# Performance work log

Measured on AMD Instinct MI355X. Metric: run time of the kernel, lower is better.

The kernel has to match this reference:

```python
import jax, jax.numpy as jnp
import numpy as np

M = 4096      # dictionary_size
D = 64        # feature dim
YD = 4        # output dim (y_dim)
FF = 0.999    # forgetting_factor
REG = 1e-2    # regularisation
JITTER = 1e-10
LS = 8.0      # RBF lengthscale


def rbf(a, b):
    # squared-distance RBF Gram via the ||a||^2 + ||b||^2 - 2ab^T identity
    a2 = jnp.sum(a * a, -1)[:, None]
    b2 = jnp.sum(b * b, -1)[None, :]
    d2 = jnp.maximum(a2 + b2 - 2.0 * (a @ b.T), 0.0)
    return jnp.exp(-d2 / (2.0 * LS * LS))


def setup_inputs() -> dict:
    key = jax.random.key(0)
    ks = jax.random.split(key, 7)
    return {
        'dictionary': jax.random.normal(ks[0], (M, D), jnp.float32),
        'mu': jax.random.normal(ks[1], (YD, M, 1), jnp.float32),
        'sigma': jax.random.normal(ks[2], (M, M), jnp.float32),
        'Q': jax.random.normal(ks[3], (M, M), jnp.float32),
        'x': jax.random.normal(ks[4], (D,), jnp.float32),
        'y': jax.random.normal(ks[5], (YD,), jnp.float32),
        'noise_num': jax.random.uniform(ks[6], (YD, 1, 1), jnp.float32),
        'noise_den': jnp.ones((1,), jnp.float32),
        'time_index': jnp.arange(M, dtype=jnp.float32),
        't': M,
    }


def reference(dictionary, mu, sigma, Q, x, y, noise_num, noise_den, time_index, t):
    alloc = time_index >= 0.0                      # (M,) bool: allocated slots
    y_ = y[:, None, None]                          # (YD,1,1)

    # --- B2P forgetting ---
    Kdd = rbf(dictionary, dictionary) * (alloc[:, None] * alloc[None, :])
    sig = FF * sigma + (1.0 - FF) * Kdd
    mu_f = jnp.sqrt(FF) * mu

    # --- kernel evals for new sample ---
    K_dx = rbf(dictionary, x[None, :]) * alloc[:, None]   # (M,1)
    K_xx = rbf(x[None, :], x[None, :]) + JITTER           # (1,1)

    q_ = Q @ K_dx                                         # (M,1)
    pu = jnp.maximum(K_xx - K_dx.T @ q_, 0.0)             # projection uncertainty (1,1)
    h_ = sig @ q_                                         # (M,1)
    npv = jnp.maximum(pu + q_.T @ h_, 0.0)                # noiseless predictive var (1,1)
    pred_mean = q_.T @ mu_f                               # (YD,1,1) via batched matmul
    pv = REG + npv

    # --- augmented (M+1) state ---
    p_ = jnp.concatenate((h_, npv), axis=-2)              # (M+1,1)
    mu_a = jnp.concatenate((mu_f, pred_mean), axis=-2) + (y_ - pred_mean) / pv * p_
    sig_a = jnp.block([[sig, h_], [h_.T, npv]]) - (p_ @ p_.T) / pv
    p2 = jnp.concatenate((q_, -jnp.ones((1, 1), q_.dtype)), axis=0)
    Q_a = jnp.pad(Q, ((0, 1), (0, 1))) + (p2 @ p2.T) / pu

    nnum = noise_num + FF * (y_ - pred_mean) ** 2 / pv
    nden = noise_den + FF

    # --- pruning criterion ---
    x_alloc = jnp.concatenate((alloc, jnp.ones((1,), bool)))

    def crit_low(_):
        return jnp.concatenate((jnp.ones((M, 1), Q_a.dtype), jnp.zeros((1, 1), Q_a.dtype)))

    def crit_mse(_):
        dq = jnp.where(~x_alloc, jnp.inf, jnp.diag(Q_a))
        errors = Q_a @ mu_a / dq[:, None]                 # (YD,M+1,1)
        return jnp.abs(errors).sum(-3)                    # (M+1,1)

    criterion = jax.lax.cond(pu.squeeze() < JITTER, crit_low, crit_mse, None)
    prune = jnp.argmin(criterion)
    denom = jnp.where(~x_alloc[prune], jnp.inf, Q_a[prune, prune])

    # swap (prune <-> last) permutation, then drop last row/col
    perm = jnp.arange(M + 1)
    perm = jnp.where(perm == prune, M, jnp.where(perm == M, prune, perm))

    Q_r = Q_a[perm, :]                                    # row swap
    Qs = Q_r[:-1, prune]                                  # column `prune` after row swap
    Q_n = Q_r[:, perm][:M, :M] - jnp.outer(Qs, Qs) / denom

    mu_n = mu_a[:, perm, :][:, :M, :]
    sig_n = sig_a[perm, :][:, perm][:M, :M]

    dict_n = dictionary.at[prune].set(x)
    ti_n = time_index.at[prune].set(jnp.asarray(t, time_index.dtype))
    alloc_n = ti_n >= 0.0
    sig_n = (alloc_n[:, None] * alloc_n[None, :]) * sig_n
    mu_n = jnp.where((ti_n < 0.0)[:, None], 0.0, mu_n)

    return (mu_n, sig_n, Q_n, dict_n, ti_n, nnum, nden)
```

## Files before the change

kernel.cpp:

```cpp
#include <hip/hip_runtime.h>
#include <math.h>

#define Mn 4096
#define Dn 64
#define MUA_STRIDE 4104

#define OFF_A2   0
#define OFF_CRIT 0
#define OFF_K    4096
#define OFF_Q    8192
#define OFF_H    12288
#define OFF_MUA  16384
#define OFF_QS   32800
#define OFF_QSD  36896
#define SC_PU    40992
#define SC_INVPU 40993
#define SC_NPV   40994
#define SC_PV    40995
#define SC_INVPV 40996
#define SC_DENOM 40997
#define SC_PRUNE 40998

#define O_MU   0
#define O_SIG  16384
#define O_Q    16793600
#define O_DICT 33570816
#define O_TI   33832960
#define O_NNUM 33837056
#define O_NDEN 33837060

__device__ __forceinline__ float waveReduceSum(float v) {
#pragma unroll
    for (int o = 32; o > 0; o >>= 1) v += __shfl_down(v, o);
    return v;
}

__global__ void k1_prep(const float* __restrict__ dict, const float* __restrict__ x,
                        const float* __restrict__ ti, float* __restrict__ ws) {
    int row  = blockIdx.x * 4 + (threadIdx.x >> 6);
    int lane = threadIdx.x & 63;
    float d  = dict[row * Dn + lane];
    float xv = x[lane];
    float a2 = waveReduceSum(d * d);
    float x2 = waveReduceSum(xv * xv);
    float dx = waveReduceSum(d * xv);
    if (lane == 0) {
        ws[OFF_A2 + row] = a2;
        float d2 = fmaxf(a2 + x2 - 2.0f * dx, 0.0f);
        float kv = expf(d2 * (-1.0f / 128.0f));
        ws[OFF_K + row] = (ti[row] >= 0.0f) ? kv : 0.0f;
    }
}

__global__ void k2_q(const float* __restrict__ Q, float* __restrict__ ws) {
    __shared__ float red[4];
    const int row = blockIdx.x;
    const int tid = threadIdx.x;
    const float4* Qr = (const float4*)(Q + (size_t)row * Mn);
    const float4* kv = (const float4*)(ws + OFF_K);
    float s = 0.0f;
#pragma unroll
    for (int it = 0; it < 4; ++it) {
        int u = tid + it * 256;
        float4 a = Qr[u], b = kv[u];
        s += a.x * b.x + a.y * b.y + a.z * b.z + a.w * b.w;
    }
    s = waveReduceSum(s);
    if ((tid & 63) == 0) red[tid >> 6] = s;
    __syncthreads();
    if (tid == 0) {
        ws[OFF_Q + row] = red[0] + red[1] + red[2] + red[3];
        ws[OFF_H + row] = 0.0f;
    }
}

__global__ __launch_bounds__(256, 4) void k3_sig_h(
        const float* __restrict__ dict, const float* __restrict__ sigma,
        const float* __restrict__ ti, float* __restrict__ ws, float* __restrict__ out) {
    __shared__ __align__(16) float At[64 * 68];
    __shared__ __align__(16) float Bt[64 * 68];
    __shared__ float hred[64 * 16];
    const int tid = threadIdx.x;
    const int tx = tid & 15, ty = tid >> 4;
    const int r0 = blockIdx.y * 64;
    const int cchunk = blockIdx.x * 256;
    const int pidx = ((tid & 15) << 4) | (tid >> 4);

#pragma unroll
    for (int l = 0; l < 4; ++l) {
        int u = pidx + l * 256;
        int row = u >> 4;
        int col = (u & 15) << 2;
        float4 v = *(const float4*)(dict + (size_t)(r0 + row) * Dn + col);
        At[(col + 0) * 68 + row] = v.x;
        At[(col + 1) * 68 + row] = v.y;
        At[(col + 2) * 68 + row] = v.z;
        At[(col + 3) * 68 + row] = v.w;
    }

    float a2i[4], ali[4];
#pragma unroll
    for (int r = 0; r < 4; ++r) {
        int gi = r0 + ty * 4 + r;
        a2i[r] = ws[OFF_A2 + gi];
        ali[r] = (ti[gi] >= 0.0f) ? 1.0f : 0.0f;
    }

    float hacc[4] = {0.f, 0.f, 0.f, 0.f};

    for (int ct = 0; ct < 4; ++ct) {
        const int c0 = cchunk + ct * 64;
        __syncthreads();
#pragma unroll
        for (int l = 0; l < 4; ++l) {
            int u = pidx + l * 256;
            int row = u >> 4;
            int col = (u & 15) << 2;
            float4 v = *(const float4*)(dict + (size_t)(c0 + row) * Dn + col);
            Bt[(col + 0) * 68 + row] = v.x;
            Bt[(col + 1) * 68 + row] = v.y;
            Bt[(col + 2) * 68 + row] = v.z;
            Bt[(col + 3) * 68 + row] = v.w;
        }
        __syncthreads();

        float acc[4][4];
#pragma unroll
        for (int r = 0; r < 4; ++r)
#pragma unroll
            for (int c = 0; c < 4; ++c) acc[r][c] = 0.0f;

#pragma unroll
        for (int kk = 0; kk < 64; ++kk) {
            float4 av = *(const float4*)(At + kk * 68 + (ty << 2));
            float4 bv = *(const float4*)(Bt + kk * 68 + (tx << 2));
            acc[0][0] = fmaf(av.x, bv.x, acc[0][0]);
            acc[0][1] = fmaf(av.x, bv.y, acc[0][1]);
            acc[0][2] = fmaf(av.x, bv.z, acc[0][2]);
            acc[0][3] = fmaf(av.x, bv.w, acc[0][3]);
            acc[1][0] = fmaf(av.y, bv.x, acc[1][0]);
            acc[1][1] = fmaf(av.y, bv.y, acc[1][1]);
            acc[1][2] = fmaf(av.y, bv.z, acc[1][2]);
            acc[1][3] = fmaf(av.y, bv.w, acc[1][3]);
            acc[2][0] = fmaf(av.z, bv.x, acc[2][0]);
            acc[2][1] = fmaf(av.z, bv.y, acc[2][1]);
            acc[2][2] = fmaf(av.z, bv.z, acc[2][2]);
            acc[2][3] = fmaf(av.z, bv.w, acc[2][3]);
            acc[3][0] = fmaf(av.w, bv.x, acc[3][0]);
            acc[3][1] = fmaf(av.w, bv.y, acc[3][1]);
            acc[3][2] = fmaf(av.w, bv.z, acc[3][2]);
            acc[3][3] = fmaf(av.w, bv.w, acc[3][3]);
        }

        const int j = c0 + tx * 4;
        const float4 a2j4 = *(const float4*)(ws + OFF_A2 + j);
        const float4 qj4  = *(const float4*)(ws + OFF_Q + j);
        const float4 tj4  = *(const float4*)(ti + j);
        float a2j[4] = {a2j4.x, a2j4.y, a2j4.z, a2j4.w};
        float qj[4]  = {qj4.x, qj4.y, qj4.z, qj4.w};
        float alj[4] = {tj4.x >= 0.f ? 1.f : 0.f, tj4.y >= 0.f ? 1.f : 0.f,
                        tj4.z >= 0.f ? 1.f : 0.f, tj4.w >= 0.f ? 1.f : 0.f};

#pragma unroll
        for (int r = 0; r < 4; ++r) {
            const int gi = r0 + ty * 4 + r;
            const size_t off = (size_t)gi * Mn + j;
            const float4 sg = *(const float4*)(sigma + off);
            float sv[4] = {sg.x, sg.y, sg.z, sg.w};
            float res[4];
#pragma unroll
            for (int c = 0; c < 4; ++c) {
                float d2 = fmaxf(a2i[r] + a2j[c] - 2.0f * acc[r][c], 0.0f);
                float kv = __expf(d2 * (-1.0f / 128.0f)) * ali[r] * alj[c];
                res[c] = 0.999f * sv[c] + 0.001f * kv;
                hacc[r] += res[c] * qj[c];
            }
            float4 o = {res[0], res[1], res[2], res[3]};
            *(float4*)(out + O_SIG + off) = o;
        }
    }

    __syncthreads();
#pragma unroll
    for (int r = 0; r < 4; ++r) hred[(ty * 4 + r) * 16 + tx] = hacc[r];
    __syncthreads();
    if (tid < 64) {
        float s = 0.0f;
#pragma unroll
        for (int c = 0; c < 16; ++c) s += hred[tid * 16 + c];
        atomicAdd(ws + OFF_H + r0 + tid, s);
    }
}

__device__ __forceinline__ float blockReduce1024(float v, float* sred) {
    v = waveReduceSum(v);
    int tid = threadIdx.x;
    __syncthreads();
    if ((tid & 63) == 0) sred[tid >> 6] = v;
    __syncthreads();
    float r = 0.0f;
    if (tid == 0) {
#pragma unroll
        for (int i = 0; i < 16; ++i) r += sred[i];
    }
    return r;
}

__global__ __launch_bounds__(1024) void k4_scalars(
        const float* __restrict__ mu, const float* __restrict__ y,
        const float* __restrict__ nn, const float* __restrict__ nd,
        float* __restrict__ ws, float* __restrict__ out) {
    __shared__ float sred[16];
    __shared__ float sb[8];
    const int tid = threadIdx.x;
    const float* k = ws + OFF_K;
    const float* q = ws + OFF_Q;
    const float* h = ws + OFF_H;
    float kq = 0, qh = 0, p0 = 0, p1 = 0, p2 = 0, p3 = 0;
    for (int i = tid; i < Mn; i += 1024) {
        float qi = q[i];
        kq += k[i] * qi;
        qh += qi * h[i];
        p0 += qi * mu[0 * Mn + i];
        p1 += qi * mu[1 * Mn + i];
        p2 += qi * mu[2 * Mn + i];
        p3 += qi * mu[3 * Mn + i];
    }
    float rkq = blockReduce1024(kq, sred);
    float rqh = blockReduce1024(qh, sred);
    float r0 = blockReduce1024(p0, sred);
    float r1 = blockReduce1024(p1, sred);
    float r2 = blockReduce1024(p2, sred);
    float r3 = blockReduce1024(p3, sred);
    if (tid == 0) {
        const float sf = sqrtf(0.999f);
        float pu  = fmaxf(1.0f - rkq, 0.0f);
        float npv = fmaxf(pu + rqh, 0.0f);
        float pv  = 0.01f + npv;
        ws[SC_PU] = pu;
        ws[SC_INVPU] = 1.0f / pu;
        ws[SC_NPV] = npv;
        ws[SC_PV] = pv;
        ws[SC_INVPV] = 1.0f / pv;
        float pm[4] = {sf * r0, sf * r1, sf * r2, sf * r3};
#pragma unroll
        for (int yd = 0; yd < 4; ++yd) {
            float yv = y[yd];
            float dy = yv - pm[yd];
            float dl = dy / pv;
            sb[yd] = dl;
            ws[OFF_MUA + yd * MUA_STRIDE + Mn] = pm[yd] + dl * npv;
            out[O_NNUM + yd] = nn[yd] + 0.999f * (dy * dy) / pv;
        }
        out[O_NDEN] = nd[0] + 0.999f;
    }
    __syncthreads();
    const float sf = sqrtf(0.999f);
    float d0 = sb[0], d1 = sb[1], d2 = sb[2], d3 = sb[3];
    for (int i = tid; i < Mn; i += 1024) {
        float hi = h[i];
        ws[OFF_MUA + 0 * MUA_STRIDE + i] = sf * mu[0 * Mn + i] + d0 * hi;
        ws[OFF_MUA + 1 * MUA_STRIDE + i] = sf * mu[1 * Mn + i] + d1 * hi;
        ws[OFF_MUA + 2 * MUA_STRIDE + i] = sf * mu[2 * Mn + i] + d2 * hi;
        ws[OFF_MUA + 3 * MUA_STRIDE + i] = sf * mu[3 * Mn + i] + d3 * hi;
    }
}

__global__ __launch_bounds__(256) void k5_crit(const float* __restrict__ Q,
                                               const float* __restrict__ ti,
                                               float* __restrict__ ws) {
    __shared__ float sred[4][4];
    const int row = blockIdx.x;
    const int tid = threadIdx.x;
    const float pu = ws[SC_PU];
    if (pu < 1e-10f) {
        if (tid == 0) ws[OFF_CRIT + row] = (row < Mn) ? 1.0f : 0.0f;
        return;
    }
    const float inv_pu = ws[SC_INVPU];
    const bool rin = (row < Mn);
    const float p2i = rin ? ws[OFF_Q + row] : -1.0f;
    const float4* q4  = (const float4*)(ws + OFF_Q);
    const float4* Qr4 = (const float4*)(Q + (size_t)row * Mn);
    const float* mua = ws + OFF_MUA;
    float n0 = 0, n1 = 0, n2 = 0, n3 = 0;
#pragma unroll
    for (int it = 0; it < 4; ++it) {
        int u = tid + it * 256;
        float4 qv = q4[u];
        float4 base = rin ? Qr4[u] : make_float4(0.f, 0.f, 0.f, 0.f);
        float4 qa;
        qa.x = base.x + p2i * qv.x * inv_pu;
        qa.y = base.y + p2i * qv.y * inv_pu;
        qa.z = base.z + p2i * qv.z * inv_pu;
        qa.w = base.w + p2i * qv.w * inv_pu;
        const float4 m0 = *(const float4*)(mua + 0 * MUA_STRIDE + u * 4);
        const float4 m1 = *(const float4*)(mua + 1 * MUA_STRIDE + u * 4);
        const float4 m2 = *(const float4*)(mua + 2 * MUA_STRIDE + u * 4);
        const float4 m3 = *(const float4*)(mua + 3 * MUA_STRIDE + u * 4);
        n0 += qa.x * m0.x + qa.y * m0.y + qa.z * m0.z + qa.w * m0.w;
        n1 += qa.x * m1.x + qa.y * m1.y + qa.z * m1.z + qa.w * m1.w;
        n2 += qa.x * m2.x + qa.y * m2.y + qa.z * m2.z + qa.w * m2.w;
        n3 += qa.x * m3.x + qa.y * m3.y + qa.z * m3.z + qa.w * m3.w;
    }
    n0 = waveReduceSum(n0);
    n1 = waveReduceSum(n1);
    n2 = waveReduceSum(n2);
    n3 = waveReduceSum(n3);
    if ((tid & 63) == 0) {
        int w = tid >> 6;
        sred[w][0] = n0; sred[w][1] = n1; sred[w][2] = n2; sred[w][3] = n3;
    }
    __syncthreads();
    if (tid == 0) {
        float t0 = 0, t1 = 0, t2 = 0, t3 = 0;
#pragma unroll
        for (int w = 0; w < 4; ++w) {
            t0 += sred[w][0]; t1 += sred[w][1]; t2 += sred[w][2]; t3 += sred[w][3];
        }
        float qaM = -p2i * inv_pu;
        t0 += qaM * mua[0 * MUA_STRIDE + Mn];
        t1 += qaM * mua[1 * MUA_STRIDE + Mn];
        t2 += qaM * mua[2 * MUA_STRIDE + Mn];
        t3 += qaM * mua[3 * MUA_STRIDE + Mn];
        bool xa = rin ? (ti[row] >= 0.0f) : true;
        float crit = 0.0f;
        if (xa) {
            float dq = rin ? (Q[(size_t)row * Mn + row] + p2i * p2i * inv_pu) : inv_pu;
            crit = fabsf(t0 / dq) + fabsf(t1 / dq) + fabsf(t2 / dq) + fabsf(t3 / dq);
        }
        ws[OFF_CRIT + row] = crit;
    }
}

__global__ __launch_bounds__(1024) void k6_argmin(const float* __restrict__ Q,
                                                  const float* __restrict__ ti,
                                                  float* __restrict__ ws) {
    __shared__ float sval[1024];
    __shared__ int   sidx[1024];
    const int tid = threadIdx.x;
    float bv = INFINITY;
    int bi = Mn + 1;
    for (int i = tid; i <= Mn; i += 1024) {
        float v = ws[OFF_CRIT + i];
        if (v < bv) { bv = v; bi = i; }
    }
    sval[tid] = bv; sidx[tid] = bi;
    __syncthreads();
    for (int s = 512; s > 0; s >>= 1) {
        if (tid < s) {
            float ov = sval[tid + s]; int oi = sidx[tid + s];
            if (ov < sval[tid] || (ov == sval[tid] && oi < sidx[tid])) {
                sval[tid] = ov; sidx[tid] = oi;
            }
        }
        __syncthreads();
    }
    if (tid == 0) {
        int prune = sidx[0];
        ((int*)ws)[SC_PRUNE] = prune;
        float inv_pu = ws[SC_INVPU];
        bool xa = (prune == Mn) ? true : (ti[prune] >= 0.0f);
        float qap;
        if (prune < Mn) {
            float qp = ws[OFF_Q + prune];
            qap = Q[(size_t)prune * Mn + prune] + qp * qp * inv_pu;
        } else {
            qap = inv_pu;
        }
        ws[SC_DENOM] = xa ? qap : INFINITY;
    }
}

__global__ void k6b_vec(const float* __restrict__ Q, const float* __restrict__ dict,
                        const float* __restrict__ x, const float* __restrict__ ti,
                        const int* __restrict__ tptr, float* __restrict__ ws,
                        float* __restrict__ out) {
    const int tid = blockIdx.x * 256 + threadIdx.x;
    const int prune = ((const int*)ws)[SC_PRUNE];
    const int row = tid >> 6, col = tid & 63;
    out[O_DICT + tid] = (row == prune) ? x[col] : dict[tid];
    if (tid < Mn) {
        float tv = ti[tid];
        if (tid == prune) {
            int raw = *tptr;
            tv = (raw >= 0 && raw < (1 << 30)) ? (float)raw : __int_as_float(raw);
        }
        out[O_TI + tid] = tv;
        const float inv_pu = ws[SC_INVPU];
        const float denom  = ws[SC_DENOM];
        const float p2p = (prune < Mn) ? ws[OFF_Q + prune] : -1.0f;
        float qs;
        if (tid == prune) {
            qs = -p2p * inv_pu;
        } else {
            float base = (prune < Mn) ? Q[(size_t)tid * Mn + prune] : 0.0f;
            qs = base + ws[OFF_Q + tid] * p2p * inv_pu;
        }
        ws[OFF_QS + tid] = qs;
        ws[OFF_QSD + tid] = qs / denom;
    }
}

__global__ void k7_qn(const float* __restrict__ Q, float* __restrict__ out,
                      const float* __restrict__ ws) {
    const int i = blockIdx.x;
    const int tid = threadIdx.x;
    const int prune = ((const int*)ws)[SC_PRUNE];
    const float inv_pu = ws[SC_INVPU];
    const int pi = (i == prune) ? Mn : i;
    const bool piok = (pi < Mn);
    const float p2i = piok ? ws[OFF_Q + pi] : -1.0f;
    const float qsi = ws[OFF_QS + i];
    const float4* Qr4  = (const float4*)(Q + (size_t)pi * Mn);
    const float4* q4   = (const float4*)(ws + OFF_Q);
    const float4* qsd4 = (const float4*)(ws + OFF_QSD);
    float4* o4 = (float4*)(out + O_Q + (size_t)i * Mn);
#pragma unroll
    for (int it = 0; it < 4; ++it) {
        int u = tid + it * 256;
        float4 base = piok ? Qr4[u] : make_float4(0.f, 0.f, 0.f, 0.f);
        float4 p2j = q4[u];
        if ((prune >> 2) == u) {
            int c = prune & 3;
            ((float*)&p2j)[c] = -1.0f;
            ((float*)&base)[c] = 0.0f;
        }
        float4 d = qsd4[u];
        float4 r;
        r.x = base.x + p2i * p2j.x * inv_pu - qsi * d.x;
        r.y = base.y + p2i * p2j.y * inv_pu - qsi * d.y;
        r.z = base.z + p2i * p2j.z * inv_pu - qsi * d.z;
        r.w = base.w + p2i * p2j.w * inv_pu - qsi * d.w;
        o4[u] = r;
    }
}

__global__ void k8_sign(float* __restrict__ out, const float* __restrict__ ws) {
    const int i = blockIdx.x;
    const int tid = threadIdx.x;
    const int prune = ((const int*)ws)[SC_PRUNE];
    const float inv_pv = ws[SC_INVPV];
    const float npv = ws[SC_NPV];
    const bool ip = (i == prune);
    const float ai = (out[O_TI + i] >= 0.0f) ? 1.0f : 0.0f;
    const float hi = ws[OFF_H + i];
    const float p_i = ip ? npv : hi;
    const float4* h4  = (const float4*)(ws + OFF_H);
    const float4* ti4 = (const float4*)(out + O_TI);
    float4* s4 = (float4*)(out + O_SIG + (size_t)i * Mn);
#pragma unroll
    for (int it = 0; it < 4; ++it) {
        int u = tid + it * 256;
        float4 sv = s4[u];
        float4 hj = h4[u];
        float4 tv = ti4[u];
        float pj[4] = {hj.x, hj.y, hj.z, hj.w};
        float bs[4];
        if (ip) { bs[0] = hj.x; bs[1] = hj.y; bs[2] = hj.z; bs[3] = hj.w; }
        else    { bs[0] = sv.x; bs[1] = sv.y; bs[2] = sv.z; bs[3] = sv.w; }
        if ((prune >> 2) == u) {
            int c = prune & 3;
            pj[c] = npv;
            bs[c] = ip ? npv : hi;
        }
        float aj[4] = {tv.x >= 0.f ? 1.f : 0.f, tv.y >= 0.f ? 1.f : 0.f,
                       tv.z >= 0.f ? 1.f : 0.f, tv.w >= 0.f ? 1.f : 0.f};
        float4 r;
        r.x = ai * aj[0] * (bs[0] - p_i * pj[0] * inv_pv);
        r.y = ai * aj[1] * (bs[1] - p_i * pj[1] * inv_pv);
        r.z = ai * aj[2] * (bs[2] - p_i * pj[2] * inv_pv);
        r.w = ai * aj[3] * (bs[3] - p_i * pj[3] * inv_pv);
        s4[u] = r;
    }
}

__global__ void k9_mun(float* __restrict__ out, const float* __restrict__ ws) {
    const int idx = blockIdx.x * 256 + threadIdx.x;
    const int prune = ((const int*)ws)[SC_PRUNE];
    const int yd = idx >> 12;
    const int i  = idx & (Mn - 1);
    float tin = out[O_TI + i];
    float v;
    if (tin < 0.0f) v = 0.0f;
    else v = ws[OFF_MUA + yd * MUA_STRIDE + ((i == prune) ? Mn : i)];
    out[O_MU + idx] = v;
}

extern "C" void kernel_launch(void* const* d_in, const int* in_sizes, int n_in,
                              void* d_out, int out_size, void* d_ws, size_t ws_size,
                              hipStream_t stream) {
    const float* dict  = (const float*)d_in[0];
    const float* mu    = (const float*)d_in[1];
    const float* sigma = (const float*)d_in[2];
    const float* Q     = (const float*)d_in[3];
    const float* x     = (const float*)d_in[4];
    const float* y     = (const float*)d_in[5];
    const float* nn    = (const float*)d_in[6];
    const float* nd    = (const float*)d_in[7];
    const float* ti    = (const float*)d_in[8];
    const int*   tptr  = (const int*)d_in[9];
    float* out = (float*)d_out;
    float* ws  = (float*)d_ws;

    k1_prep<<<1024, 256, 0, stream>>>(dict, x, ti, ws);
    k2_q<<<4096, 256, 0, stream>>>(Q, ws);
    k3_sig_h<<<dim3(16, 64), 256, 0, stream>>>(dict, sigma, ti, ws, out);
    k4_scalars<<<1, 1024, 0, stream>>>(mu, y, nn, nd, ws, out);
    k5_crit<<<4097, 256, 0, stream>>>(Q, ti, ws);
    k6_argmin<<<1, 1024, 0, stream>>>(Q, ti, ws);
    k6b_vec<<<1024, 256, 0, stream>>>(Q, dict, x, ti, tptr, ws, out);
    k7_qn<<<4096, 256, 0, stream>>>(Q, out, ws);
    k8_sign<<<4096, 256, 0, stream>>>(out, ws);
    k9_mun<<<64, 256, 0, stream>>>(out, ws);
}
```

Measured before the change: 345.2 us.

## Fuse final Q/sigma/mu update kernels and prefetch dictionary tiles in k3

Merges the three tail kernels (Q update, sigma update, mu update) into one launch per row, which removes two kernel launches and their scheduling gaps. In k3, each block now covers half as many column tiles, so the grid doubles and more blocks are resident. The next dictionary tile is also register-prefetched while the current one is stored to shared memory, to hide global load latency. The risks are extra register pressure from the prefetch buffer and the A-tile load being repeated across twice as many blocks.

```diff
diff --git a/kernel.cpp b/kernel.cpp
--- a/kernel.cpp
+++ b/kernel.cpp
@@ -83,8 +83,10 @@
     const int tid = threadIdx.x;
     const int tx = tid & 15, ty = tid >> 4;
     const int r0 = blockIdx.y * 64;
-    const int cchunk = blockIdx.x * 256;
+    const int cchunk = blockIdx.x * 128;
     const int pidx = ((tid & 15) << 4) | (tid >> 4);
+    const int prow = pidx >> 4;
+    const int pcol = (pidx & 15) << 2;
 
 #pragma unroll
     for (int l = 0; l < 4; ++l) {
@@ -108,7 +110,15 @@
 
     float hacc[4] = {0.f, 0.f, 0.f, 0.f};
 
-    for (int ct = 0; ct < 4; ++ct) {
+    float4 pre[4];
+#pragma unroll
+    for (int l = 0; l < 4; ++l) {
+        int row = (pidx + l * 256) >> 4;
+        int col = ((pidx + l * 256) & 15) << 2;
+        pre[l] = *(const float4*)(dict + (size_t)(cchunk + row) * Dn + col);
+    }
+
+    for (int ct = 0; ct < 2; ++ct) {
         const int c0 = cchunk + ct * 64;
         __syncthreads();
 #pragma unroll
@@ -116,11 +126,19 @@
             int u = pidx + l * 256;
             int row = u >> 4;
             int col = (u & 15) << 2;
-            float4 v = *(const float4*)(dict + (size_t)(c0 + row) * Dn + col);
-            Bt[(col + 0) * 68 + row] = v.x;
-            Bt[(col + 1) * 68 + row] = v.y;
-            Bt[(col + 2) * 68 + row] = v.z;
-            Bt[(col + 3) * 68 + row] = v.w;
+            Bt[(col + 0) * 68 + row] = pre[l].x;
+            Bt[(col + 1) * 68 + row] = pre[l].y;
+            Bt[(col + 2) * 68 + row] = pre[l].z;
+            Bt[(col + 3) * 68 + row] = pre[l].w;
+        }
+        if (ct < 1) {
+            const int c1 = cchunk + (ct + 1) * 64;
+#pragma unroll
+            for (int l = 0; l < 4; ++l) {
+                int row = (pidx + l * 256) >> 4;
+                int col = ((pidx + l * 256) & 15) << 2;
+                pre[l] = *(const float4*)(dict + (size_t)(c1 + row) * Dn + col);
+            }
         }
         __syncthreads();
 
@@ -402,12 +420,16 @@
     }
 }
 
-__global__ void k7_qn(const float* __restrict__ Q, float* __restrict__ out,
-                      const float* __restrict__ ws) {
+__global__ __launch_bounds__(256) void k7_fused(const float* __restrict__ Q,
+                                                float* __restrict__ out,
+                                                const float* __restrict__ ws) {
     const int i = blockIdx.x;
     const int tid = threadIdx.x;
     const int prune = ((const int*)ws)[SC_PRUNE];
     const float inv_pu = ws[SC_INVPU];
+    const float inv_pv = ws[SC_INVPV];
+    const float npv = ws[SC_NPV];
+
     const int pi = (i == prune) ? Mn : i;
     const bool piok = (pi < Mn);
     const float p2i = piok ? ws[OFF_Q + pi] : -1.0f;
@@ -434,14 +456,7 @@
         r.w = base.w + p2i * p2j.w * inv_pu - qsi * d.w;
         o4[u] = r;
     }
-}
-
-__global__ void k8_sign(float* __restrict__ out, const float* __restrict__ ws) {
-    const int i = blockIdx.x;
-    const int tid = threadIdx.x;
-    const int prune = ((const int*)ws)[SC_PRUNE];
-    const float inv_pv = ws[SC_INVPV];
-    const float npv = ws[SC_NPV];
+
     const bool ip = (i == prune);
     const float ai = (out[O_TI + i] >= 0.0f) ? 1.0f : 0.0f;
     const float hi = ws[OFF_H + i];
@@ -473,18 +488,14 @@
         r.w = ai * aj[3] * (bs[3] - p_i * pj[3] * inv_pv);
         s4[u] = r;
     }
-}
-
-__global__ void k9_mun(float* __restrict__ out, const float* __restrict__ ws) {
-    const int idx = blockIdx.x * 256 + threadIdx.x;
-    const int prune = ((const int*)ws)[SC_PRUNE];
-    const int yd = idx >> 12;
-    const int i  = idx & (Mn - 1);
-    float tin = out[O_TI + i];
-    float v;
-    if (tin < 0.0f) v = 0.0f;
-    else v = ws[OFF_MUA + yd * MUA_STRIDE + ((i == prune) ? Mn : i)];
-    out[O_MU + idx] = v;
+
+    if (tid < 4) {
+        float tin = out[O_TI + i];
+        float v;
+        if (tin < 0.0f) v = 0.0f;
+        else v = ws[OFF_MUA + tid * MUA_STRIDE + (ip ? Mn : i)];
+        out[O_MU + tid * Mn + i] = v;
+    }
 }
 
 extern "C" void kernel_launch(void* const* d_in, const int* in_sizes, int n_in,
@@ -505,12 +516,10 @@
 
     k1_prep<<<1024, 256, 0, stream>>>(dict, x, ti, ws);
     k2_q<<<4096, 256, 0, stream>>>(Q, ws);
-    k3_sig_h<<<dim3(16, 64), 256, 0, stream>>>(dict, sigma, ti, ws, out);
+    k3_sig_h<<<dim3(32, 64), 256, 0, stream>>>(dict, sigma, ti, ws, out);
     k4_scalars<<<1, 1024, 0, stream>>>(mu, y, nn, nd, ws, out);
     k5_crit<<<4097, 256, 0, stream>>>(Q, ti, ws);
     k6_argmin<<<1, 1024, 0, stream>>>(Q, ti, ws);
     k6b_vec<<<1024, 256, 0, stream>>>(Q, dict, x, ti, tptr, ws, out);
-    k7_qn<<<4096, 256, 0, stream>>>(Q, out, ws);
-    k8_sign<<<4096, 256, 0, stream>>>(out, ws);
-    k9_mun<<<64, 256, 0, stream>>>(out, ws);
-}
+    k7_fused<<<4096, 256, 0, stream>>>(Q, out, ws);
+}
```

After: 337.6 us. 1.02x faster.
